# Performance work log

Hardware: AMD Instinct MI355X
Metric: run time of the kernel (lower is better)

The kernel has to match this reference:

```python
import jax, jax.numpy as jnp
import numpy as np

N_NODES = 50000
N_EDGES = 800000
N_GRAPHS = 64


def setup_inputs() -> dict:
    key = jax.random.key(0)
    ks = jax.random.split(key, 12)

    def w(k, shape):
        fan_in = shape[0]
        return jax.random.normal(k, shape, dtype=jnp.float32) / np.sqrt(fan_in)

    x = jax.random.normal(ks[0], (N_NODES, 6), dtype=jnp.float32)
    edge_index = jax.random.randint(ks[1], (2, N_EDGES), 0, N_NODES, dtype=jnp.int64)
    batch = jnp.sort(jax.random.randint(ks[2], (N_NODES,), 0, N_GRAPHS, dtype=jnp.int64))
    return {
        "x": x,
        "edge_index": edge_index,
        "batch": batch,
        "W_in": w(ks[3], (6, 64)),
        "b_in": jnp.zeros((64,), jnp.float32),
        "W1": w(ks[4], (64, 128)),
        "b1": jnp.zeros((128,), jnp.float32),
        "W2": w(ks[5], (128, 128)),
        "b2": jnp.zeros((128,), jnp.float32),
        "Wp": w(ks[6], (256, 256)),
        "bp": jnp.zeros((256,), jnp.float32),
    }


def reference(x, edge_index, batch, W_in, b_in, W1, b1, W2, b2, Wp, bp):
    n = x.shape[0]
    self_loop = jnp.arange(n, dtype=edge_index.dtype)
    src = jnp.concatenate([edge_index[0], self_loop])  # [E+N]
    dst = jnp.concatenate([edge_index[1], self_loop])
    # GCN symmetric normalization with self-loops (PyG GCNConv default)
    deg = jax.ops.segment_sum(jnp.ones_like(dst, x.dtype), dst, num_segments=n)
    dinv = jax.lax.rsqrt(deg)  # deg >= 1 because of self-loops
    norm = (dinv[src] * dinv[dst])[:, None]  # [E+N, 1]

    def gcn(h, W, b):
        hw = h @ W                       # linear first, like GCNConv
        msg = hw[src] * norm             # gather + normalize per edge
        return jax.ops.segment_sum(msg, dst, num_segments=n) + b

    h = x @ W_in + b_in                  # input_projection
    h = jax.nn.relu(gcn(h, W1, b1))      # relu(gnn1(...))
    h = jax.nn.relu(gcn(h, W2, b2))      # relu(gnn2(...))

    # global mean / max pooling over batch segments
    counts = jax.ops.segment_sum(jnp.ones((n,), h.dtype), batch, num_segments=N_GRAPHS)
    h_mean = jax.ops.segment_sum(h, batch, num_segments=N_GRAPHS) / jnp.maximum(counts, 1.0)[:, None]
    h_max = jax.ops.segment_max(h, batch, num_segments=N_GRAPHS)
    h_max = jnp.where(counts[:, None] > 0, h_max, 0.0)
    h_graph = jnp.concatenate([h_mean, h_max], axis=1)  # [G, 256]

    # projection MLP: Linear + ReLU (Dropout is identity in eval)
    return jax.nn.relu(h_graph @ Wp + bp)
```

## Files before the change

kernel.cpp:

```cpp
#include <hip/hip_runtime.h>
#include <hip/hip_fp16.h>

#define N_NODES 50000
#define N_EDGES 800000
#define N_GRAPHS 64
#define N_PAD 50048

#define CB 256
#define EPB (N_EDGES / CB)
#define NBUCKET ((N_NODES + 255) / 256)

typedef _Float16 f16x8 __attribute__((ext_vector_type(8)));
typedef float f32x4 __attribute__((ext_vector_type(4)));

struct H8 { __half2 a, b, c, d; };


__global__ void k_prep(const float* __restrict__ W1, const float* __restrict__ W2,
                       _Float16* __restrict__ Wt1, _Float16* __restrict__ Wt2,
                       float* psum, float* pmax, int* totals) {
    int idx = blockIdx.x * blockDim.x + threadIdx.x;
    if (idx < 128 * 64) {
        int n = idx >> 6, k = idx & 63;
        Wt1[idx] = (_Float16)W1[k * 128 + n];
    } else if (idx < 128 * 64 + 128 * 128) {
        int j = idx - 128 * 64;
        int n = j >> 7, k = j & 127;
        Wt2[j] = (_Float16)W2[k * 128 + n];
    }
    if (idx < N_GRAPHS * 128) { psum[idx] = 0.f; pmax[idx] = 0.f; }
    if (idx < 256) totals[idx] = 0;
}


__global__ __launch_bounds__(256) void k_coarse_hist(const int* __restrict__ dst,
                                                     int* __restrict__ totals) {
    __shared__ int hist[NBUCKET];
    int t = threadIdx.x, b = blockIdx.x;
    for (int i = t; i < NBUCKET; i += 256) hist[i] = 0;
    __syncthreads();
    int e0 = b * EPB;
    for (int e = e0 + t; e < e0 + EPB; e += 256)
        atomicAdd(&hist[dst[e] >> 8], 1);
    __syncthreads();
    for (int i = t; i < NBUCKET; i += 256)
        if (hist[i] > 0) atomicAdd(&totals[i], hist[i]);
}

__global__ void k_bucket_scan(const int* __restrict__ totals, int* __restrict__ bucket_base,
                              int* __restrict__ gcursor, const int* __restrict__ batch,
                              float* __restrict__ pcnt) {
    __shared__ int sh[256];
    int t = threadIdx.x;
    int v = (t < NBUCKET) ? totals[t] : 0;
    sh[t] = v;
    __syncthreads();
    for (int off = 1; off < 256; off <<= 1) {
        int u = (t >= off) ? sh[t - off] : 0;
        __syncthreads();
        sh[t] += u;
        __syncthreads();
    }
    if (t < NBUCKET) {
        int base = sh[t] - v;
        bucket_base[t] = base;
        gcursor[t] = base;
    }
    if (t == 0) bucket_base[NBUCKET] = N_EDGES;
    if (t <= N_GRAPHS) {
        int lo = 0, hi = N_NODES;
        while (lo < hi) {
            int mid = (lo + hi) >> 1;
            if (batch[mid] < t) lo = mid + 1; else hi = mid;
        }
        sh[t] = lo;
    }
    __syncthreads();
    if (t < N_GRAPHS) pcnt[t] = (float)(sh[t + 1] - sh[t]);
}

__global__ __launch_bounds__(256) void k_coarse_scatter(
        const int* __restrict__ src, const int* __restrict__ dst,
        int* __restrict__ gcursor, unsigned int* __restrict__ esort) {
    __shared__ int cur[NBUCKET];
    int t = threadIdx.x, b = blockIdx.x;
    for (int i = t; i < NBUCKET; i += 256) cur[i] = 0;
    __syncthreads();
    int e0 = b * EPB;
    for (int e = e0 + t; e < e0 + EPB; e += 256)
        atomicAdd(&cur[dst[e] >> 8], 1);
    __syncthreads();
    for (int i = t; i < NBUCKET; i += 256) {
        int cnt = cur[i];
        cur[i] = (cnt > 0) ? atomicAdd(&gcursor[i], cnt) : 0;
    }
    __syncthreads();
    for (int e = e0 + t; e < e0 + EPB; e += 256) {
        int d = dst[e];
        int slot = atomicAdd(&cur[d >> 8], 1);
        esort[slot] = ((unsigned)(d & 255) << 16) | (unsigned)src[e];
    }
}

__global__ __launch_bounds__(256) void k_fine_fill_proj(
        const unsigned int* __restrict__ esort, const int* __restrict__ bucket_base,
        int* __restrict__ col, int* __restrict__ row_ptr, float* __restrict__ dinv,
        const float* __restrict__ x, const float* __restrict__ W_in,
        const float* __restrict__ b_in, _Float16* __restrict__ g0) {
    __shared__ int hist[256];
    __shared__ int sc[256];
    __shared__ int cur[256];
    int t = threadIdx.x, b = blockIdx.x;
    hist[t] = 0;
    __syncthreads();
    int base = bucket_base[b], end = bucket_base[b + 1];
    for (int e = base + t; e < end; e += 256)
        atomicAdd(&hist[(esort[e] >> 16) & 255], 1);
    __syncthreads();
    int v = hist[t];
    sc[t] = v;
    __syncthreads();
    for (int off = 1; off < 256; off <<= 1) {
        int u = (t >= off) ? sc[t - off] : 0;
        __syncthreads();
        sc[t] += u;
        __syncthreads();
    }
    int start = base + sc[t] - v;
    cur[t] = start;
    int node = b * 256 + t;
    float di = rsqrtf((float)(v + 1));
    if (node < N_NODES) {
        row_ptr[node] = start;
        dinv[node] = di;
    }
    if (b == 0 && t == 0) row_ptr[N_NODES] = N_EDGES;
    __syncthreads();
    for (int e = base + t; e < end; e += 256) {
        unsigned pk = esort[e];
        int slot = atomicAdd(&cur[(pk >> 16) & 255], 1);
        col[slot] = (int)(pk & 0xffffu);
    }
    if (node < N_NODES) {
        float xr[6];
#pragma unroll
        for (int k = 0; k < 6; k++) xr[k] = x[node * 6 + k];
#pragma unroll
        for (int oc = 0; oc < 8; oc++) {
            f16x8 o;
#pragma unroll
            for (int j = 0; j < 8; j++) {
                int cl = oc * 8 + j;
                float acc = b_in[cl];
#pragma unroll
                for (int k = 0; k < 6; k++) acc += xr[k] * W_in[k * 64 + cl];
                o[j] = (_Float16)(acc * di);
            }
            *(f16x8*)&g0[(size_t)node * 64 + oc * 8] = o;
        }
    }
}

template <int K, int ROWS, bool HALF_OUT, bool POOL>
__global__ __launch_bounds__(256, 8) void k_gnn(
        const _Float16* __restrict__ g, const int* __restrict__ row_ptr,
        const int* __restrict__ col, const _Float16* __restrict__ Wt_h,
        const float* __restrict__ b, const float* __restrict__ dinv,
        void* __restrict__ outp, const int* __restrict__ batch,
        float* __restrict__ psum, float* __restrict__ pmax, int n) {
    constexpr int KP = K + 8;
    constexpr int TPR = 256 / ROWS;
    constexpr int CO8 = K / 8;
    static_assert(K / TPR == 8, "8 channels per gather thread");
    constexpr int S_BYTES = ROWS * KP * 2;
    constexpr int H_BYTES = POOL ? ROWS * 128 * 4 : 0;
    constexpr int SMEM = S_BYTES > H_BYTES ? S_BYTES : H_BYTES;
    __shared__ __align__(16) char smem[SMEM];
    _Float16* Sl = (_Float16*)smem;
    float* Hs = (float*)smem;
    int t = threadIdx.x;

    {
        int row_local = t / TPR;
        int ck = t % TPR;
        int row = blockIdx.x * ROWS + row_local;
        float accA[8] = {};
        float accB[8] = {};
        const H8* gb = (const H8*)g;
        auto addv = [](float* acc, H8 v) {
            float2 f;
            f = __half22float2(v.a); acc[0] += f.x; acc[1] += f.y;
            f = __half22float2(v.b); acc[2] += f.x; acc[3] += f.y;
            f = __half22float2(v.c); acc[4] += f.x; acc[5] += f.y;
            f = __half22float2(v.d); acc[6] += f.x; acc[7] += f.y;
        };
        if (row < n) {
            addv(accA, gb[(size_t)row * CO8 + ck]);
            int e = row_ptr[row], e1 = row_ptr[row + 1];
            for (; e + 3 < e1; e += 4) {
                int c0 = col[e], c1 = col[e + 1], c2 = col[e + 2], c3 = col[e + 3];
                H8 v0 = gb[(size_t)c0 * CO8 + ck];
                H8 v1 = gb[(size_t)c1 * CO8 + ck];
                H8 v2 = gb[(size_t)c2 * CO8 + ck];
                H8 v3 = gb[(size_t)c3 * CO8 + ck];
                addv(accA, v0);
                addv(accB, v1);
                addv(accA, v2);
                addv(accB, v3);
            }
            if (e + 1 < e1) {
                H8 v0 = gb[(size_t)col[e] * CO8 + ck];
                H8 v1 = gb[(size_t)col[e + 1] * CO8 + ck];
                addv(accA, v0);
                addv(accB, v1);
                e += 2;
            }
            if (e < e1) addv(accA, gb[(size_t)col[e] * CO8 + ck]);
        }
        f16x8 o;
#pragma unroll
        for (int q = 0; q < 8; q++) o[q] = (_Float16)(accA[q] + accB[q]);
        *(f16x8*)&Sl[row_local * KP + ck * 8] = o;
    }
    __syncthreads();

    int wave = t >> 6;
    int lane = t & 63;
    int m = lane & 15;
    int quad = lane >> 4;
    constexpr int COLT = (ROWS == 16) ? 2 : 4;
    int col_base = (ROWS == 16) ? wave * 32 : (wave >> 1) * 64;
    int rbl = (ROWS == 16) ? 0 : (wave & 1) * 16;
    int wrow0 = blockIdx.x * ROWS + rbl;

    f32x4 acc[COLT] = {};
#pragma unroll
    for (int k0 = 0; k0 < K; k0 += 32) {
        f16x8 a = *(const f16x8*)&Sl[(rbl + m) * KP + k0 + quad * 8];
#pragma unroll
        for (int ct = 0; ct < COLT; ct++) {
            f16x8 bw = *(const f16x8*)(Wt_h + (size_t)(col_base + ct * 16 + m) * K + k0 + quad * 8);
            acc[ct] = __builtin_amdgcn_mfma_f32_16x16x32_f16(a, bw, acc[ct], 0, 0, 0);
        }
    }

    if (!POOL) {
#pragma unroll
        for (int r = 0; r < 4; r++) {
            int row = wrow0 + quad * 4 + r;
            if (row < n) {
                float di = dinv[row];
#pragma unroll
                for (int ct = 0; ct < COLT; ct++) {
                    int colb = col_base + ct * 16 + m;
                    float v = fmaxf(di * acc[ct][r] + b[colb], 0.f);
                    if (HALF_OUT)
                        ((_Float16*)outp)[(size_t)row * 128 + colb] = (_Float16)(v * di);
                    else
                        ((float*)outp)[(size_t)row * 128 + colb] = v;
                }
            }
        }
    } else {
        __syncthreads();
#pragma unroll
        for (int r = 0; r < 4; r++) {
            int rl = quad * 4 + r;
            int row = wrow0 + rl;
            float di = (row < n) ? dinv[row] : 0.f;
#pragma unroll
            for (int ct = 0; ct < COLT; ct++) {
                int colb = col_base + ct * 16 + m;
                float v = fmaxf(di * acc[ct][r] + b[colb], 0.f);
                Hs[rl * 128 + colb] = (row < n) ? v : 0.f;
            }
        }
        __syncthreads();
        if (t < 128) {
            int colb = t;
            int row0b = blockIdx.x * ROWS;
            float s = 0.f, mx = 0.f;
            int gcur = batch[row0b < n ? row0b : (n - 1)];
            for (int rl = 0; rl < ROWS; rl++) {
                int row = row0b + rl;
                if (row >= n) break;
                int gi = batch[row];
                if (gi != gcur) {
                    atomicAdd(&psum[gcur * 128 + colb], s);
                    atomicMax((int*)&pmax[gcur * 128 + colb], __float_as_int(mx));
                    s = 0.f; mx = 0.f; gcur = gi;
                }
                float v = Hs[rl * 128 + colb];
                s += v;
                mx = fmaxf(mx, v);
            }
            atomicAdd(&psum[gcur * 128 + colb], s);
            atomicMax((int*)&pmax[gcur * 128 + colb], __float_as_int(mx));
        }
    }
}


__global__ void k_final(const float* __restrict__ psum, const float* __restrict__ pmax,
                        const float* __restrict__ pcnt, const float* __restrict__ Wp,
                        const float* __restrict__ bp, float* __restrict__ out) {
    int t = blockIdx.x * blockDim.x + threadIdx.x;
    if (t >= N_GRAPHS * 256) return;
    int g = t >> 8, j = t & 255;
    float inv = 1.0f / fmaxf(pcnt[g], 1.0f);
    float acc = bp[j];
#pragma unroll 4
    for (int k = 0; k < 128; k++) acc += (psum[g * 128 + k] * inv) * Wp[k * 256 + j];
#pragma unroll 4
    for (int k = 0; k < 128; k++) acc += pmax[g * 128 + k] * Wp[(128 + k) * 256 + j];
    out[t] = fmaxf(acc, 0.f);
}

extern "C" void kernel_launch(void* const* d_in, const int* in_sizes, int n_in,
                              void* d_out, int out_size, void* d_ws, size_t ws_size,
                              hipStream_t stream) {
    const int N = N_NODES, E = N_EDGES;
    const float* x    = (const float*)d_in[0];
    const int*   ei   = (const int*)d_in[1];
    const int*   src  = ei;
    const int*   dst  = ei + E;
    const int*   batch= (const int*)d_in[2];
    const float* W_in = (const float*)d_in[3];
    const float* b_in = (const float*)d_in[4];
    const float* W1   = (const float*)d_in[5];
    const float* b1   = (const float*)d_in[6];
    const float* W2   = (const float*)d_in[7];
    const float* b2   = (const float*)d_in[8];
    const float* Wp   = (const float*)d_in[9];
    const float* bp   = (const float*)d_in[10];
    float* out = (float*)d_out;

    char* p = (char*)d_ws;
    int* totals      = (int*)p;   p += 256 * 4;
    int* bucket_base = (int*)p;   p += 256 * 4;
    int* gcursor     = (int*)p;   p += 256 * 4;
    int* row_ptr     = (int*)p;   p += (N_PAD + 64) * 4;
    int* col         = (int*)p;   p += (size_t)N_EDGES * 4;
    unsigned* esort  = (unsigned*)p; p += (size_t)N_EDGES * 4;
    float* dinv      = (float*)p; p += N_PAD * 4;
    _Float16* Wt1    = (_Float16*)p; p += 128 * 64 * 2;
    _Float16* Wt2    = (_Float16*)p; p += 128 * 128 * 2;
    _Float16* g0h    = (_Float16*)p; p += (size_t)N_PAD * 64 * 2;
    _Float16* g1h    = (_Float16*)p; p += (size_t)N_PAD * 128 * 2;
    float* psum      = (float*)p; p += N_GRAPHS * 128 * 4;
    float* pmax      = (float*)p; p += N_GRAPHS * 128 * 4;
    float* pcnt      = (float*)p;

    const int TB = 256;
    dim3 blk(TB);

    k_prep<<<(128 * 64 + 128 * 128 + TB - 1) / TB, blk, 0, stream>>>(
        W1, W2, Wt1, Wt2, psum, pmax, totals);

    k_coarse_hist<<<CB, blk, 0, stream>>>(dst, totals);
    k_bucket_scan<<<1, blk, 0, stream>>>(totals, bucket_base, gcursor, batch, pcnt);
    k_coarse_scatter<<<CB, blk, 0, stream>>>(src, dst, gcursor, esort);
    k_fine_fill_proj<<<NBUCKET, blk, 0, stream>>>(esort, bucket_base, col, row_ptr, dinv,
                                                  x, W_in, b_in, g0h);

    k_gnn<64, 32, true, false><<<(N + 31) / 32, blk, 0, stream>>>(
        g0h, row_ptr, col, Wt1, b1, dinv, g1h, nullptr, nullptr, nullptr, N);

    k_gnn<128, 16, false, true><<<(N + 15) / 16, blk, 0, stream>>>(
        g1h, row_ptr, col, Wt2, b2, dinv, nullptr, batch, psum, pmax, N);

    k_final<<<(N_GRAPHS * 256 + TB - 1) / TB, blk, 0, stream>>>(psum, pmax, pcnt, Wp, bp, out);
}
```

Baseline: 205.9 us.

## Fuse CSR build stages into one cooperative kernel with grid syncs

Four graph-building launches (coarse histogram, bucket scan, coarse scatter, fine fill plus input projection) become one cooperative kernel that uses grid.sync() between phases. Each block keeps its edge slice in shared memory so dst and src are read only once, and it uses per-wave histograms to reduce shared-atomic contention. The goal is to cut launch overhead and repeated global reads. In exchange it adds grid-wide barriers and a large shared-memory footprint per block, which could limit co-residency for the 256-block cooperative launch.

```diff
diff --git a/kernel.cpp b/kernel.cpp
--- a/kernel.cpp
+++ b/kernel.cpp
@@ -1,5 +1,8 @@
 #include <hip/hip_runtime.h>
 #include <hip/hip_fp16.h>
+#include <hip/hip_cooperative_groups.h>
+
+namespace cg = cooperative_groups;
 
 #define N_NODES 50000
 #define N_EDGES 800000
@@ -18,7 +21,7 @@
 
 __global__ void k_prep(const float* __restrict__ W1, const float* __restrict__ W2,
                        _Float16* __restrict__ Wt1, _Float16* __restrict__ Wt2,
-                       float* psum, float* pmax, int* totals) {
+                       float* psum, float* pmax, int* totals, int* gcursor) {
     int idx = blockIdx.x * blockDim.x + threadIdx.x;
     if (idx < 128 * 64) {
         int n = idx >> 6, k = idx & 63;
@@ -29,95 +32,48 @@
         Wt2[j] = (_Float16)W2[k * 128 + n];
     }
     if (idx < N_GRAPHS * 128) { psum[idx] = 0.f; pmax[idx] = 0.f; }
-    if (idx < 256) totals[idx] = 0;
-}
-
-
-__global__ __launch_bounds__(256) void k_coarse_hist(const int* __restrict__ dst,
-                                                     int* __restrict__ totals) {
-    __shared__ int hist[NBUCKET];
-    int t = threadIdx.x, b = blockIdx.x;
-    for (int i = t; i < NBUCKET; i += 256) hist[i] = 0;
-    __syncthreads();
-    int e0 = b * EPB;
-    for (int e = e0 + t; e < e0 + EPB; e += 256)
-        atomicAdd(&hist[dst[e] >> 8], 1);
-    __syncthreads();
-    for (int i = t; i < NBUCKET; i += 256)
-        if (hist[i] > 0) atomicAdd(&totals[i], hist[i]);
-}
-
-__global__ void k_bucket_scan(const int* __restrict__ totals, int* __restrict__ bucket_base,
-                              int* __restrict__ gcursor, const int* __restrict__ batch,
-                              float* __restrict__ pcnt) {
-    __shared__ int sh[256];
-    int t = threadIdx.x;
-    int v = (t < NBUCKET) ? totals[t] : 0;
-    sh[t] = v;
-    __syncthreads();
-    for (int off = 1; off < 256; off <<= 1) {
-        int u = (t >= off) ? sh[t - off] : 0;
-        __syncthreads();
-        sh[t] += u;
-        __syncthreads();
-    }
-    if (t < NBUCKET) {
-        int base = sh[t] - v;
-        bucket_base[t] = base;
-        gcursor[t] = base;
-    }
-    if (t == 0) bucket_base[NBUCKET] = N_EDGES;
-    if (t <= N_GRAPHS) {
-        int lo = 0, hi = N_NODES;
-        while (lo < hi) {
-            int mid = (lo + hi) >> 1;
-            if (batch[mid] < t) lo = mid + 1; else hi = mid;
-        }
-        sh[t] = lo;
-    }
-    __syncthreads();
-    if (t < N_GRAPHS) pcnt[t] = (float)(sh[t + 1] - sh[t]);
-}
-
-__global__ __launch_bounds__(256) void k_coarse_scatter(
+    if (idx < 256) { totals[idx] = 0; gcursor[idx] = 0; }
+}
+
+
+__global__ __launch_bounds__(256) void k_build(
         const int* __restrict__ src, const int* __restrict__ dst,
-        int* __restrict__ gcursor, unsigned int* __restrict__ esort) {
-    __shared__ int cur[NBUCKET];
-    int t = threadIdx.x, b = blockIdx.x;
-    for (int i = t; i < NBUCKET; i += 256) cur[i] = 0;
-    __syncthreads();
-    int e0 = b * EPB;
-    for (int e = e0 + t; e < e0 + EPB; e += 256)
-        atomicAdd(&cur[dst[e] >> 8], 1);
-    __syncthreads();
-    for (int i = t; i < NBUCKET; i += 256) {
-        int cnt = cur[i];
-        cur[i] = (cnt > 0) ? atomicAdd(&gcursor[i], cnt) : 0;
-    }
-    __syncthreads();
-    for (int e = e0 + t; e < e0 + EPB; e += 256) {
-        int d = dst[e];
-        int slot = atomicAdd(&cur[d >> 8], 1);
-        esort[slot] = ((unsigned)(d & 255) << 16) | (unsigned)src[e];
-    }
-}
-
-__global__ __launch_bounds__(256) void k_fine_fill_proj(
-        const unsigned int* __restrict__ esort, const int* __restrict__ bucket_base,
-        int* __restrict__ col, int* __restrict__ row_ptr, float* __restrict__ dinv,
+        int* __restrict__ totals, int* __restrict__ gcursor,
+        unsigned int* __restrict__ esort, int* __restrict__ col,
+        int* __restrict__ row_ptr, float* __restrict__ dinv,
         const float* __restrict__ x, const float* __restrict__ W_in,
-        const float* __restrict__ b_in, _Float16* __restrict__ g0) {
+        const float* __restrict__ b_in, _Float16* __restrict__ g0,
+        const int* __restrict__ batch, float* __restrict__ pcnt) {
+    __shared__ int lsrc[EPB];
+    __shared__ int ldst[EPB];
+    __shared__ int hist4[4][NBUCKET];
     __shared__ int hist[256];
     __shared__ int sc[256];
     __shared__ int cur[256];
+    cg::grid_group grid = cg::this_grid();
     int t = threadIdx.x, b = blockIdx.x;
-    hist[t] = 0;
-    __syncthreads();
-    int base = bucket_base[b], end = bucket_base[b + 1];
-    for (int e = base + t; e < end; e += 256)
-        atomicAdd(&hist[(esort[e] >> 16) & 255], 1);
-    __syncthreads();
-    int v = hist[t];
+    int wv = t >> 6;
+
+    if (t < NBUCKET) {
+        hist4[0][t] = 0; hist4[1][t] = 0; hist4[2][t] = 0; hist4[3][t] = 0;
+    }
+    __syncthreads();
+    int e0 = b * EPB;
+    for (int i = t; i < EPB; i += 256) {
+        int d = dst[e0 + i];
+        lsrc[i] = src[e0 + i];
+        ldst[i] = d;
+        atomicAdd(&hist4[wv][d >> 8], 1);
+    }
+    __syncthreads();
+    if (t < NBUCKET) {
+        int c = hist4[0][t] + hist4[1][t] + hist4[2][t] + hist4[3][t];
+        hist[t] = c;
+        if (c > 0) atomicAdd(&totals[t], c);
+    }
+    grid.sync();
+
+    int v = (t < NBUCKET) ? totals[t] : 0;
     sc[t] = v;
     __syncthreads();
     for (int off = 1; off < 256; off <<= 1) {
@@ -126,38 +82,81 @@
         sc[t] += u;
         __syncthreads();
     }
-    int start = base + sc[t] - v;
-    cur[t] = start;
-    int node = b * 256 + t;
-    float di = rsqrtf((float)(v + 1));
-    if (node < N_NODES) {
-        row_ptr[node] = start;
-        dinv[node] = di;
-    }
-    if (b == 0 && t == 0) row_ptr[N_NODES] = N_EDGES;
-    __syncthreads();
-    for (int e = base + t; e < end; e += 256) {
-        unsigned pk = esort[e];
-        int slot = atomicAdd(&cur[(pk >> 16) & 255], 1);
-        col[slot] = (int)(pk & 0xffffu);
-    }
-    if (node < N_NODES) {
-        float xr[6];
-#pragma unroll
-        for (int k = 0; k < 6; k++) xr[k] = x[node * 6 + k];
-#pragma unroll
-        for (int oc = 0; oc < 8; oc++) {
-            f16x8 o;
-#pragma unroll
-            for (int j = 0; j < 8; j++) {
-                int cl = oc * 8 + j;
-                float acc = b_in[cl];
-#pragma unroll
-                for (int k = 0; k < 6; k++) acc += xr[k] * W_in[k * 64 + cl];
-                o[j] = (_Float16)(acc * di);
-            }
-            *(f16x8*)&g0[(size_t)node * 64 + oc * 8] = o;
-        }
+    if (t < NBUCKET) {
+        int cnt = hist[t];
+        int base = sc[t] - v;
+        cur[t] = (cnt > 0) ? (base + atomicAdd(&gcursor[t], cnt)) : 0;
+    }
+    __syncthreads();
+
+    for (int i = t; i < EPB; i += 256) {
+        int d = ldst[i];
+        int slot = atomicAdd(&cur[d >> 8], 1);
+        esort[slot] = ((unsigned)(d & 255) << 16) | (unsigned)lsrc[i];
+    }
+    int mybase = (b < NBUCKET) ? (sc[b] - totals[b]) : 0;
+    int myend  = (b < NBUCKET) ? sc[b] : 0;
+    grid.sync();
+
+    if (b < NBUCKET) {
+        hist[t] = 0;
+        __syncthreads();
+        for (int e = mybase + t; e < myend; e += 256)
+            atomicAdd(&hist[(esort[e] >> 16) & 255], 1);
+        __syncthreads();
+        int fv = hist[t];
+        sc[t] = fv;
+        __syncthreads();
+        for (int off = 1; off < 256; off <<= 1) {
+            int u = (t >= off) ? sc[t - off] : 0;
+            __syncthreads();
+            sc[t] += u;
+            __syncthreads();
+        }
+        int start = mybase + sc[t] - fv;
+        cur[t] = start;
+        int node = b * 256 + t;
+        float di = rsqrtf((float)(fv + 1));
+        if (node < N_NODES) {
+            row_ptr[node] = start;
+            dinv[node] = di;
+        }
+        __syncthreads();
+        for (int e = mybase + t; e < myend; e += 256) {
+            unsigned pk = esort[e];
+            int slot = atomicAdd(&cur[(pk >> 16) & 255], 1);
+            col[slot] = (int)(pk & 0xffffu);
+        }
+        if (node < N_NODES) {
+            float xr[6];
+#pragma unroll
+            for (int k = 0; k < 6; k++) xr[k] = x[node * 6 + k];
+#pragma unroll
+            for (int oc = 0; oc < 8; oc++) {
+                f16x8 o;
+#pragma unroll
+                for (int j = 0; j < 8; j++) {
+                    int cl = oc * 8 + j;
+                    float acc = b_in[cl];
+#pragma unroll
+                    for (int k = 0; k < 6; k++) acc += xr[k] * W_in[k * 64 + cl];
+                    o[j] = (_Float16)(acc * di);
+                }
+                *(f16x8*)&g0[(size_t)node * 64 + oc * 8] = o;
+            }
+        }
+    } else if (b == NBUCKET) {
+        if (t == 0) row_ptr[N_NODES] = N_EDGES;
+        if (t <= N_GRAPHS) {
+            int lo = 0, hi = N_NODES;
+            while (lo < hi) {
+                int mid = (lo + hi) >> 1;
+                if (batch[mid] < t) lo = mid + 1; else hi = mid;
+            }
+            sc[t] = lo;
+        }
+        __syncthreads();
+        if (t < N_GRAPHS) pcnt[t] = (float)(sc[t + 1] - sc[t]);
     }
 }
 
@@ -350,18 +349,23 @@
     float* psum      = (float*)p; p += N_GRAPHS * 128 * 4;
     float* pmax      = (float*)p; p += N_GRAPHS * 128 * 4;
     float* pcnt      = (float*)p;
+    (void)bucket_base;
 
     const int TB = 256;
     dim3 blk(TB);
 
     k_prep<<<(128 * 64 + 128 * 128 + TB - 1) / TB, blk, 0, stream>>>(
-        W1, W2, Wt1, Wt2, psum, pmax, totals);
-
-    k_coarse_hist<<<CB, blk, 0, stream>>>(dst, totals);
-    k_bucket_scan<<<1, blk, 0, stream>>>(totals, bucket_base, gcursor, batch, pcnt);
-    k_coarse_scatter<<<CB, blk, 0, stream>>>(src, dst, gcursor, esort);
-    k_fine_fill_proj<<<NBUCKET, blk, 0, stream>>>(esort, bucket_base, col, row_ptr, dinv,
-                                                  x, W_in, b_in, g0h);
+        W1, W2, Wt1, Wt2, psum, pmax, totals, gcursor);
+
+    {
+        void* args[] = {
+            (void*)&src, (void*)&dst, (void*)&totals, (void*)&gcursor,
+            (void*)&esort, (void*)&col, (void*)&row_ptr, (void*)&dinv,
+            (void*)&x, (void*)&W_in, (void*)&b_in, (void*)&g0h,
+            (void*)&batch, (void*)&pcnt
+        };
+        hipLaunchCooperativeKernel((void*)k_build, dim3(CB), blk, args, 0, stream);
+    }
 
     k_gnn<64, 32, true, false><<<(N + 31) / 32, blk, 0, stream>>>(
         g0h, row_ptr, col, Wt1, b1, dinv, g1h, nullptr, nullptr, nullptr, N);
```

Result: slower. 274.6 us (+33.4%).

## Split second GCN layer into standalone gather kernel and GEMM+pool kernel

Applied to the files above, without the earlier changes.

The fused gather+MFMA+pooling kernel for layer 2 becomes two kernels. A pure gather kernel writes aggregated fp16 features to a new workspace buffer, and a GEMM+pool kernel reads them back, applies W2, bias and ReLU, and does the segment pooling. The split lets the gather run without shared memory or barriers for better occupancy and latency hiding. In exchange it adds an extra launch and a round trip of the N×128 fp16 intermediate through global memory.

```diff
diff --git a/kernel.cpp b/kernel.cpp
--- a/kernel.cpp
+++ b/kernel.cpp
@@ -161,23 +161,17 @@
     }
 }
 
-template <int K, int ROWS, bool HALF_OUT, bool POOL>
+template <int K, int ROWS, bool HALF_OUT>
 __global__ __launch_bounds__(256, 8) void k_gnn(
         const _Float16* __restrict__ g, const int* __restrict__ row_ptr,
         const int* __restrict__ col, const _Float16* __restrict__ Wt_h,
         const float* __restrict__ b, const float* __restrict__ dinv,
-        void* __restrict__ outp, const int* __restrict__ batch,
-        float* __restrict__ psum, float* __restrict__ pmax, int n) {
+        void* __restrict__ outp, int n) {
     constexpr int KP = K + 8;
     constexpr int TPR = 256 / ROWS;
     constexpr int CO8 = K / 8;
     static_assert(K / TPR == 8, "8 channels per gather thread");
-    constexpr int S_BYTES = ROWS * KP * 2;
-    constexpr int H_BYTES = POOL ? ROWS * 128 * 4 : 0;
-    constexpr int SMEM = S_BYTES > H_BYTES ? S_BYTES : H_BYTES;
-    __shared__ __align__(16) char smem[SMEM];
-    _Float16* Sl = (_Float16*)smem;
-    float* Hs = (float*)smem;
+    __shared__ __align__(16) _Float16 Sl[ROWS * KP];
     int t = threadIdx.x;
 
     {
@@ -244,59 +238,143 @@
         }
     }
 
-    if (!POOL) {
-#pragma unroll
-        for (int r = 0; r < 4; r++) {
-            int row = wrow0 + quad * 4 + r;
-            if (row < n) {
-                float di = dinv[row];
-#pragma unroll
-                for (int ct = 0; ct < COLT; ct++) {
-                    int colb = col_base + ct * 16 + m;
-                    float v = fmaxf(di * acc[ct][r] + b[colb], 0.f);
-                    if (HALF_OUT)
-                        ((_Float16*)outp)[(size_t)row * 128 + colb] = (_Float16)(v * di);
-                    else
-                        ((float*)outp)[(size_t)row * 128 + colb] = v;
-                }
-            }
-        }
-    } else {
-        __syncthreads();
-#pragma unroll
-        for (int r = 0; r < 4; r++) {
-            int rl = quad * 4 + r;
-            int row = wrow0 + rl;
-            float di = (row < n) ? dinv[row] : 0.f;
+#pragma unroll
+    for (int r = 0; r < 4; r++) {
+        int row = wrow0 + quad * 4 + r;
+        if (row < n) {
+            float di = dinv[row];
 #pragma unroll
             for (int ct = 0; ct < COLT; ct++) {
                 int colb = col_base + ct * 16 + m;
                 float v = fmaxf(di * acc[ct][r] + b[colb], 0.f);
-                Hs[rl * 128 + colb] = (row < n) ? v : 0.f;
+                if (HALF_OUT)
+                    ((_Float16*)outp)[(size_t)row * 128 + colb] = (_Float16)(v * di);
+                else
+                    ((float*)outp)[(size_t)row * 128 + colb] = v;
             }
         }
-        __syncthreads();
-        if (t < 128) {
-            int colb = t;
-            int row0b = blockIdx.x * ROWS;
-            float s = 0.f, mx = 0.f;
-            int gcur = batch[row0b < n ? row0b : (n - 1)];
-            for (int rl = 0; rl < ROWS; rl++) {
-                int row = row0b + rl;
-                if (row >= n) break;
-                int gi = batch[row];
-                if (gi != gcur) {
-                    atomicAdd(&psum[gcur * 128 + colb], s);
-                    atomicMax((int*)&pmax[gcur * 128 + colb], __float_as_int(mx));
-                    s = 0.f; mx = 0.f; gcur = gi;
-                }
-                float v = Hs[rl * 128 + colb];
-                s += v;
-                mx = fmaxf(mx, v);
+    }
+}
+
+__global__ __launch_bounds__(256, 8) void k_gather128(
+        const _Float16* __restrict__ g, const int* __restrict__ row_ptr,
+        const int* __restrict__ col, _Float16* __restrict__ s, int n) {
+    constexpr int TPR = 16, CO8 = 16;
+    int idx = blockIdx.x * blockDim.x + threadIdx.x;
+    int row = idx / TPR;
+    int ck = idx % TPR;
+    if (row >= n) return;
+    float accA[8] = {};
+    float accB[8] = {};
+    const H8* gb = (const H8*)g;
+    auto addv = [](float* acc, H8 v) {
+        float2 f;
+        f = __half22float2(v.a); acc[0] += f.x; acc[1] += f.y;
+        f = __half22float2(v.b); acc[2] += f.x; acc[3] += f.y;
+        f = __half22float2(v.c); acc[4] += f.x; acc[5] += f.y;
+        f = __half22float2(v.d); acc[6] += f.x; acc[7] += f.y;
+    };
+    addv(accA, gb[(size_t)row * CO8 + ck]);
+    int e = row_ptr[row], e1 = row_ptr[row + 1];
+    for (; e + 3 < e1; e += 4) {
+        int c0 = col[e], c1 = col[e + 1], c2 = col[e + 2], c3 = col[e + 3];
+        H8 v0 = gb[(size_t)c0 * CO8 + ck];
+        H8 v1 = gb[(size_t)c1 * CO8 + ck];
+        H8 v2 = gb[(size_t)c2 * CO8 + ck];
+        H8 v3 = gb[(size_t)c3 * CO8 + ck];
+        addv(accA, v0);
+        addv(accB, v1);
+        addv(accA, v2);
+        addv(accB, v3);
+    }
+    if (e + 1 < e1) {
+        H8 v0 = gb[(size_t)col[e] * CO8 + ck];
+        H8 v1 = gb[(size_t)col[e + 1] * CO8 + ck];
+        addv(accA, v0);
+        addv(accB, v1);
+        e += 2;
+    }
+    if (e < e1) addv(accA, gb[(size_t)col[e] * CO8 + ck]);
+    f16x8 o;
+#pragma unroll
+    for (int q = 0; q < 8; q++) o[q] = (_Float16)(accA[q] + accB[q]);
+    *(f16x8*)&s[(size_t)row * 128 + ck * 8] = o;
+}
+
+__global__ __launch_bounds__(256, 8) void k_gemm_pool(
+        const _Float16* __restrict__ s, const _Float16* __restrict__ Wt_h,
+        const float* __restrict__ b, const float* __restrict__ dinv,
+        const int* __restrict__ batch, float* __restrict__ psum,
+        float* __restrict__ pmax, int n) {
+    constexpr int K = 128, ROWS = 16, KP = K + 8;
+    constexpr int S_BYTES = ROWS * KP * 2;
+    constexpr int H_BYTES = ROWS * 128 * 4;
+    constexpr int SMEM = S_BYTES > H_BYTES ? S_BYTES : H_BYTES;
+    __shared__ __align__(16) char smem[SMEM];
+    _Float16* Sl = (_Float16*)smem;
+    float* Hs = (float*)smem;
+    int t = threadIdx.x;
+
+    {
+        int rl = t >> 4, ck = t & 15;
+        int row = blockIdx.x * ROWS + rl;
+        f16x8 v = *(const f16x8*)&s[(size_t)row * K + ck * 8];
+        *(f16x8*)&Sl[rl * KP + ck * 8] = v;
+    }
+    __syncthreads();
+
+    int wave = t >> 6;
+    int lane = t & 63;
+    int m = lane & 15;
+    int quad = lane >> 4;
+    int col_base = wave * 32;
+    int wrow0 = blockIdx.x * ROWS;
+
+    f32x4 acc[2] = {};
+#pragma unroll
+    for (int k0 = 0; k0 < K; k0 += 32) {
+        f16x8 a = *(const f16x8*)&Sl[m * KP + k0 + quad * 8];
+#pragma unroll
+        for (int ct = 0; ct < 2; ct++) {
+            f16x8 bw = *(const f16x8*)(Wt_h + (size_t)(col_base + ct * 16 + m) * K + k0 + quad * 8);
+            acc[ct] = __builtin_amdgcn_mfma_f32_16x16x32_f16(a, bw, acc[ct], 0, 0, 0);
+        }
+    }
+
+    __syncthreads();
+#pragma unroll
+    for (int r = 0; r < 4; r++) {
+        int rl = quad * 4 + r;
+        int row = wrow0 + rl;
+        float di = (row < n) ? dinv[row] : 0.f;
+#pragma unroll
+        for (int ct = 0; ct < 2; ct++) {
+            int colb = col_base + ct * 16 + m;
+            float v = fmaxf(di * acc[ct][r] + b[colb], 0.f);
+            Hs[rl * 128 + colb] = (row < n) ? v : 0.f;
+        }
+    }
+    __syncthreads();
+    if (t < 128) {
+        int colb = t;
+        int row0b = blockIdx.x * ROWS;
+        float ssum = 0.f, mx = 0.f;
+        int gcur = batch[row0b < n ? row0b : (n - 1)];
+        for (int rl = 0; rl < ROWS; rl++) {
+            int row = row0b + rl;
+            if (row >= n) break;
+            int gi = batch[row];
+            if (gi != gcur) {
+                atomicAdd(&psum[gcur * 128 + colb], ssum);
+                atomicMax((int*)&pmax[gcur * 128 + colb], __float_as_int(mx));
+                ssum = 0.f; mx = 0.f; gcur = gi;
             }
-            atomicAdd(&psum[gcur * 128 + colb], s);
-            atomicMax((int*)&pmax[gcur * 128 + colb], __float_as_int(mx));
-        }
+            float v = Hs[rl * 128 + colb];
+            ssum += v;
+            mx = fmaxf(mx, v);
+        }
+        atomicAdd(&psum[gcur * 128 + colb], ssum);
+        atomicMax((int*)&pmax[gcur * 128 + colb], __float_as_int(mx));
     }
 }
 
@@ -349,7 +427,8 @@
     _Float16* g1h    = (_Float16*)p; p += (size_t)N_PAD * 128 * 2;
     float* psum      = (float*)p; p += N_GRAPHS * 128 * 4;
     float* pmax      = (float*)p; p += N_GRAPHS * 128 * 4;
-    float* pcnt      = (float*)p;
+    float* pcnt      = (float*)p; p += N_GRAPHS * 4;
+    _Float16* s2h    = (_Float16*)p; p += (size_t)N_PAD * 128 * 2;
 
     const int TB = 256;
     dim3 blk(TB);
@@ -363,11 +442,12 @@
     k_fine_fill_proj<<<NBUCKET, blk, 0, stream>>>(esort, bucket_base, col, row_ptr, dinv,
                                                   x, W_in, b_in, g0h);
 
-    k_gnn<64, 32, true, false><<<(N + 31) / 32, blk, 0, stream>>>(
-        g0h, row_ptr, col, Wt1, b1, dinv, g1h, nullptr, nullptr, nullptr, N);
-
-    k_gnn<128, 16, false, true><<<(N + 15) / 16, blk, 0, stream>>>(
-        g1h, row_ptr, col, Wt2, b2, dinv, nullptr, batch, psum, pmax, N);
+    k_gnn<64, 32, true><<<(N + 31) / 32, blk, 0, stream>>>(
+        g0h, row_ptr, col, Wt1, b1, dinv, g1h, N);
+
+    k_gather128<<<(N * 16 + TB - 1) / TB, blk, 0, stream>>>(g1h, row_ptr, col, s2h, N);
+
+    k_gemm_pool<<<(N + 15) / 16, blk, 0, stream>>>(s2h, Wt2, b2, dinv, batch, psum, pmax, N);
 
     k_final<<<(N_GRAPHS * 256 + TB - 1) / TB, blk, 0, stream>>>(psum, pmax, pcnt, Wp, bp, out);
 }
```

Measured after the change: 215.9 us. +4.9%, slower.

## Fold input projection into first GCN layer and aggregate 7-dim raw features

Applied to the files above, without the earlier changes.

Precomputes the combined W_in·W1 matrix, plus b_in·W1 as a row driven by the degree term, so that layer one aggregates only the 6 scaled input features and dinv per node instead of 64-channel fp16 hidden vectors. The neighbour gather in layer one shrinks from 128 bytes to 32 bytes per edge. The 7x128 matmul and ReLU then run after aggregation in a new fused kernel. The cost is fp32 gathers with a strided access pattern and a serial 64-term dot product per element in the prep kernel.

```diff
diff --git a/kernel.cpp b/kernel.cpp
--- a/kernel.cpp
+++ b/kernel.cpp
@@ -16,17 +16,24 @@
 struct H8 { __half2 a, b, c, d; };
 
 
-__global__ void k_prep(const float* __restrict__ W1, const float* __restrict__ W2,
-                       _Float16* __restrict__ Wt1, _Float16* __restrict__ Wt2,
+__global__ void k_prep(const float* __restrict__ W_in, const float* __restrict__ b_in,
+                       const float* __restrict__ W1, const float* __restrict__ W2,
+                       _Float16* __restrict__ Wt2, float* __restrict__ Wcz,
                        float* psum, float* pmax, int* totals) {
     int idx = blockIdx.x * blockDim.x + threadIdx.x;
-    if (idx < 128 * 64) {
-        int n = idx >> 6, k = idx & 63;
-        Wt1[idx] = (_Float16)W1[k * 128 + n];
-    } else if (idx < 128 * 64 + 128 * 128) {
-        int j = idx - 128 * 64;
-        int n = j >> 7, k = j & 127;
-        Wt2[j] = (_Float16)W2[k * 128 + n];
+    if (idx < 128 * 128) {
+        int n = idx >> 7, k = idx & 127;
+        Wt2[idx] = (_Float16)W2[k * 128 + n];
+    } else if (idx < 128 * 128 + 1024) {
+        int j = idx - 128 * 128;
+        int ch = j >> 3, k = j & 7;
+        float acc = 0.f;
+        if (k < 6) {
+            for (int q = 0; q < 64; q++) acc += W_in[k * 64 + q] * W1[q * 128 + ch];
+        } else if (k == 6) {
+            for (int q = 0; q < 64; q++) acc += b_in[q] * W1[q * 128 + ch];
+        }
+        Wcz[k * 128 + ch] = acc;
     }
     if (idx < N_GRAPHS * 128) { psum[idx] = 0.f; pmax[idx] = 0.f; }
     if (idx < 256) totals[idx] = 0;
@@ -102,11 +109,10 @@
     }
 }
 
-__global__ __launch_bounds__(256) void k_fine_fill_proj(
+__global__ __launch_bounds__(256) void k_fine_fill_p(
         const unsigned int* __restrict__ esort, const int* __restrict__ bucket_base,
         int* __restrict__ col, int* __restrict__ row_ptr, float* __restrict__ dinv,
-        const float* __restrict__ x, const float* __restrict__ W_in,
-        const float* __restrict__ b_in, _Float16* __restrict__ g0) {
+        const float* __restrict__ x, float* __restrict__ p) {
     __shared__ int hist[256];
     __shared__ int sc[256];
     __shared__ int cur[256];
@@ -133,6 +139,13 @@
     if (node < N_NODES) {
         row_ptr[node] = start;
         dinv[node] = di;
+        float pr[8];
+#pragma unroll
+        for (int k = 0; k < 6; k++) pr[k] = x[node * 6 + k] * di;
+        pr[6] = di;
+        pr[7] = 0.f;
+        *(f32x4*)&p[(size_t)node * 8] = *(f32x4*)&pr[0];
+        *(f32x4*)&p[(size_t)node * 8 + 4] = *(f32x4*)&pr[4];
     }
     if (b == 0 && t == 0) row_ptr[N_NODES] = N_EDGES;
     __syncthreads();
@@ -141,23 +154,59 @@
         int slot = atomicAdd(&cur[(pk >> 16) & 255], 1);
         col[slot] = (int)(pk & 0xffffu);
     }
-    if (node < N_NODES) {
-        float xr[6];
-#pragma unroll
-        for (int k = 0; k < 6; k++) xr[k] = x[node * 6 + k];
-#pragma unroll
-        for (int oc = 0; oc < 8; oc++) {
-            f16x8 o;
-#pragma unroll
-            for (int j = 0; j < 8; j++) {
-                int cl = oc * 8 + j;
-                float acc = b_in[cl];
-#pragma unroll
-                for (int k = 0; k < 6; k++) acc += xr[k] * W_in[k * 64 + cl];
-                o[j] = (_Float16)(acc * di);
-            }
-            *(f16x8*)&g0[(size_t)node * 64 + oc * 8] = o;
-        }
+}
+
+__global__ __launch_bounds__(256, 8) void k_agg_proj(
+        const float* __restrict__ p, const int* __restrict__ row_ptr,
+        const int* __restrict__ col, const float* __restrict__ Wcz,
+        const float* __restrict__ b1, const float* __restrict__ dinv,
+        _Float16* __restrict__ g1, int n) {
+    __shared__ float tl[32][8];
+    __shared__ float Wl[8 * 128];
+    __shared__ float bl[128];
+    int t = threadIdx.x;
+    for (int i = t; i < 1024; i += 256) Wl[i] = Wcz[i];
+    if (t < 128) bl[t] = b1[t];
+
+    int rg = t >> 3, ck = t & 7;
+    int row = blockIdx.x * 32 + rg;
+    float acc = 0.f;
+    if (row < n) {
+        acc = p[(size_t)row * 8 + ck];
+        int e = row_ptr[row], e1 = row_ptr[row + 1];
+        for (; e + 3 < e1; e += 4) {
+            int c0 = col[e], c1 = col[e + 1], c2 = col[e + 2], c3 = col[e + 3];
+            float v0 = p[(size_t)c0 * 8 + ck];
+            float v1 = p[(size_t)c1 * 8 + ck];
+            float v2 = p[(size_t)c2 * 8 + ck];
+            float v3 = p[(size_t)c3 * 8 + ck];
+            acc += (v0 + v1) + (v2 + v3);
+        }
+        for (; e < e1; e++) acc += p[(size_t)col[e] * 8 + ck];
+    }
+    tl[rg][ck] = acc;
+    __syncthreads();
+
+    int rg2 = t >> 3, oc = t & 7;
+    int row2 = blockIdx.x * 32 + rg2;
+    if (row2 < n) {
+        float tr[7];
+#pragma unroll
+        for (int k = 0; k < 7; k++) tr[k] = tl[rg2][k];
+        float di = dinv[row2];
+        f16x8 o0, o1;
+#pragma unroll
+        for (int c = 0; c < 16; c++) {
+            int ch = oc * 16 + c;
+            float z = 0.f;
+#pragma unroll
+            for (int k = 0; k < 7; k++) z += tr[k] * Wl[k * 128 + ch];
+            z = di * z + bl[ch];
+            float h = fmaxf(z, 0.f) * di;
+            if (c < 8) o0[c] = (_Float16)h; else o1[c - 8] = (_Float16)h;
+        }
+        *(f16x8*)&g1[(size_t)row2 * 128 + oc * 16] = o0;
+        *(f16x8*)&g1[(size_t)row2 * 128 + oc * 16 + 8] = o1;
     }
 }
 
@@ -335,36 +384,36 @@
     const float* bp   = (const float*)d_in[10];
     float* out = (float*)d_out;
 
-    char* p = (char*)d_ws;
-    int* totals      = (int*)p;   p += 256 * 4;
-    int* bucket_base = (int*)p;   p += 256 * 4;
-    int* gcursor     = (int*)p;   p += 256 * 4;
-    int* row_ptr     = (int*)p;   p += (N_PAD + 64) * 4;
-    int* col         = (int*)p;   p += (size_t)N_EDGES * 4;
-    unsigned* esort  = (unsigned*)p; p += (size_t)N_EDGES * 4;
-    float* dinv      = (float*)p; p += N_PAD * 4;
-    _Float16* Wt1    = (_Float16*)p; p += 128 * 64 * 2;
-    _Float16* Wt2    = (_Float16*)p; p += 128 * 128 * 2;
-    _Float16* g0h    = (_Float16*)p; p += (size_t)N_PAD * 64 * 2;
-    _Float16* g1h    = (_Float16*)p; p += (size_t)N_PAD * 128 * 2;
-    float* psum      = (float*)p; p += N_GRAPHS * 128 * 4;
-    float* pmax      = (float*)p; p += N_GRAPHS * 128 * 4;
-    float* pcnt      = (float*)p;
+    char* p8 = (char*)d_ws;
+    int* totals      = (int*)p8;   p8 += 256 * 4;
+    int* bucket_base = (int*)p8;   p8 += 256 * 4;
+    int* gcursor     = (int*)p8;   p8 += 256 * 4;
+    int* row_ptr     = (int*)p8;   p8 += (N_PAD + 64) * 4;
+    int* col         = (int*)p8;   p8 += (size_t)N_EDGES * 4;
+    unsigned* esort  = (unsigned*)p8; p8 += (size_t)N_EDGES * 4;
+    float* dinv      = (float*)p8; p8 += N_PAD * 4;
+    float* Wcz       = (float*)p8; p8 += 1024 * 4;
+    _Float16* Wt2    = (_Float16*)p8; p8 += 128 * 128 * 2;
+    float* pfeat     = (float*)p8; p8 += (size_t)N_PAD * 8 * 4;
+    _Float16* g1h    = (_Float16*)p8; p8 += (size_t)N_PAD * 128 * 2;
+    float* psum      = (float*)p8; p8 += N_GRAPHS * 128 * 4;
+    float* pmax      = (float*)p8; p8 += N_GRAPHS * 128 * 4;
+    float* pcnt      = (float*)p8;
 
     const int TB = 256;
     dim3 blk(TB);
 
-    k_prep<<<(128 * 64 + 128 * 128 + TB - 1) / TB, blk, 0, stream>>>(
-        W1, W2, Wt1, Wt2, psum, pmax, totals);
+    k_prep<<<(128 * 128 + 1024 + TB - 1) / TB, blk, 0, stream>>>(
+        W_in, b_in, W1, W2, Wt2, Wcz, psum, pmax, totals);
 
     k_coarse_hist<<<CB, blk, 0, stream>>>(dst, totals);
     k_bucket_scan<<<1, blk, 0, stream>>>(totals, bucket_base, gcursor, batch, pcnt);
     k_coarse_scatter<<<CB, blk, 0, stream>>>(src, dst, gcursor, esort);
-    k_fine_fill_proj<<<NBUCKET, blk, 0, stream>>>(esort, bucket_base, col, row_ptr, dinv,
-                                                  x, W_in, b_in, g0h);
-
-    k_gnn<64, 32, true, false><<<(N + 31) / 32, blk, 0, stream>>>(
-        g0h, row_ptr, col, Wt1, b1, dinv, g1h, nullptr, nullptr, nullptr, N);
+    k_fine_fill_p<<<NBUCKET, blk, 0, stream>>>(esort, bucket_base, col, row_ptr, dinv,
+                                               x, pfeat);
+
+    k_agg_proj<<<(N + 31) / 32, blk, 0, stream>>>(pfeat, row_ptr, col, Wcz, b1, dinv,
+                                                  g1h, N);
 
     k_gnn<128, 16, false, true><<<(N + 15) / 16, blk, 0, stream>>>(
         g1h, row_ptr, col, Wt2, b2, dinv, nullptr, batch, psum, pmax, N);
```

Measured after the change: 201.4 us. 1.02x faster.
